# Optimization experiments

Measured on AMD Instinct MI355X. Metric: run time of the kernel, lower is better.

## Reference

```python
import jax, jax.numpy as jnp
import numpy as np

B, L, C = 8, 3136, 192
HEADS, HEAD_CH = 3, 64
EPS = 1e-5


def _dwconv(x, w, s):
    # depthwise 3x3 conv, SAME padding; w: [3,3,1,C], feature_group_count=C
    return jax.lax.conv_general_dilated(
        x, w, (s, s), 'SAME',
        dimension_numbers=('NHWC', 'HWIO', 'NHWC'),
        feature_group_count=x.shape[-1])


def _proj(x, dw, scale, bias, mean, var, pw, s):
    # depthwise conv -> BN (inference, running stats) -> 1x1 pointwise conv
    h = _dwconv(x, dw, s)
    h = (h - mean) * jax.lax.rsqrt(var + EPS) * scale + bias
    return jax.lax.conv_general_dilated(
        h, pw, (1, 1), 'SAME',
        dimension_numbers=('NHWC', 'HWIO', 'NHWC'))


def setup_inputs() -> dict:
    key = jax.random.key(0)
    ks = jax.random.split(key, 7)
    d = {'x': jax.random.normal(ks[0], (B, L, C), jnp.float32)}
    for i, p in enumerate(['q', 'k', 'v']):
        d[p + '_dw'] = jax.random.normal(ks[i + 1], (3, 3, 1, C), jnp.float32) * 0.1
        d[p + '_scale'] = jnp.ones((C,), jnp.float32)
        d[p + '_bias'] = jnp.zeros((C,), jnp.float32)
        d[p + '_mean'] = jnp.zeros((C,), jnp.float32)
        d[p + '_var'] = jnp.ones((C,), jnp.float32)
        d[p + '_pw'] = jax.random.normal(ks[i + 4], (1, 1, C, HEADS * HEAD_CH), jnp.float32) * 0.05
    d['is_training'] = 0  # inference: BN uses running averages
    return d


def reference(x, q_dw, q_scale, q_bias, q_mean, q_var, q_pw,
              k_dw, k_scale, k_bias, k_mean, k_var, k_pw,
              v_dw, v_scale, v_bias, v_mean, v_var, v_pw,
              is_training):
    S = int(np.ceil(np.sqrt(L)))  # 56; L is a perfect square, so no token padding
    xi = x.reshape(B, S, S, C)
    q = _proj(xi, q_dw, q_scale, q_bias, q_mean, q_var, q_pw, 1)  # [B,56,56,192]
    k = _proj(xi, k_dw, k_scale, k_bias, k_mean, k_var, k_pw, 2)  # [B,28,28,192]
    v = _proj(xi, v_dw, v_scale, v_bias, v_mean, v_var, v_pw, 2)  # [B,28,28,192]
    q = q.reshape(B, -1, HEADS, HEAD_CH) / jnp.sqrt(jnp.float32(HEAD_CH))
    k = k.reshape(B, -1, HEADS, HEAD_CH)
    v = v.reshape(B, -1, HEADS, HEAD_CH)
    attn = jax.nn.softmax(jnp.einsum('bqhd,bkhd->bhqk', q, k), axis=-1)
    o = jnp.einsum('bhqk,bkhd->bqhd', attn, v)
    # num_heads*head_ch == out_ch -> plain head merge, no output projection
    return o.reshape(B, L, HEADS * HEAD_CH)
```

## Files before the change

### kernel.cpp

```cpp
#include <hip/hip_runtime.h>
#include <cmath>

#define EPS_BN 1e-5f

typedef __bf16 bf16;
typedef __bf16 bf16x4 __attribute__((ext_vector_type(4)));
typedef __bf16 bf16x8 __attribute__((ext_vector_type(8)));
typedef float  f32x4  __attribute__((ext_vector_type(4)));

__device__ __forceinline__ void dma16(const bf16* g, bf16* l) {
    __builtin_amdgcn_global_load_lds(
        (const __attribute__((address_space(1))) void*)g,
        (__attribute__((address_space(3))) void*)l, 16, 0, 0);
}

__global__ __launch_bounds__(256) void conv_all_kernel(
    const float* __restrict__ x,
    const float* __restrict__ qdw, const float* __restrict__ qscale,
    const float* __restrict__ qbias, const float* __restrict__ qmean,
    const float* __restrict__ qvar,
    const float* __restrict__ kdw, const float* __restrict__ kscale,
    const float* __restrict__ kbias, const float* __restrict__ kmean,
    const float* __restrict__ kvar,
    const float* __restrict__ vdw, const float* __restrict__ vscale,
    const float* __restrict__ vbias, const float* __restrict__ vmean,
    const float* __restrict__ vvar,
    const float* __restrict__ qpw, const float* __restrict__ kpw,
    const float* __restrict__ vpw,
    bf16* __restrict__ qhi, bf16* __restrict__ qlo,
    bf16* __restrict__ khi, bf16* __restrict__ klo,
    bf16* __restrict__ vhi, bf16* __restrict__ vlo,
    bf16* __restrict__ wt) {
    const int WW = 56, C = 192;
    int bid = blockIdx.x;

    if (bid < 4704) {
        int idx = bid * 256 + threadIdx.x;
        int p  = idx / 48;
        int c4 = (idx - p * 48) * 4;
        int b  = p / 3136;
        int rem = p - b * 3136;
        int oy = rem / 56;
        int ox = rem - oy * 56;
        const float* xb = x + (size_t)b * 3136 * C;

        float4 sc = *(const float4*)&qscale[c4];
        float4 vr = *(const float4*)&qvar[c4];
        float4 bi = *(const float4*)&qbias[c4];
        float4 mn = *(const float4*)&qmean[c4];
        float aA[4] = {sc.x * rsqrtf(vr.x + EPS_BN), sc.y * rsqrtf(vr.y + EPS_BN),
                       sc.z * rsqrtf(vr.z + EPS_BN), sc.w * rsqrtf(vr.w + EPS_BN)};
        float aB[4] = {bi.x - mn.x * aA[0], bi.y - mn.y * aA[1],
                       bi.z - mn.z * aA[2], bi.w - mn.w * aA[3]};
        float s[4] = {0.f, 0.f, 0.f, 0.f};
#pragma unroll
        for (int ky = 0; ky < 3; ky++) {
            int iy = oy + ky - 1;
            bool yok = (iy >= 0) && (iy < 56);
#pragma unroll
            for (int kx = 0; kx < 3; kx++) {
                int ix = ox + kx - 1;
                if (yok && ix >= 0 && ix < WW) {
                    float4 xv = *(const float4*)&xb[((size_t)iy * WW + ix) * C + c4];
                    float4 wv = *(const float4*)&qdw[(ky * 3 + kx) * C + c4];
                    s[0] += xv.x * wv.x; s[1] += xv.y * wv.y;
                    s[2] += xv.z * wv.z; s[3] += xv.w * wv.w;
                }
            }
        }
        bf16x4 hv, lv;
#pragma unroll
        for (int j = 0; j < 4; j++) {
            float av = s[j] * aA[j] + aB[j];
            bf16 hh = (bf16)av;
            hv[j] = hh;
            lv[j] = (bf16)(av - (float)hh);
        }
        *(bf16x4*)&qhi[(size_t)p * C + c4] = hv;
        *(bf16x4*)&qlo[(size_t)p * C + c4] = lv;
    } else if (bid < 5880) {
        int idx = (bid - 4704) * 256 + threadIdx.x;
        int p  = idx / 48;
        int c4 = (idx - p * 48) * 4;
        int b  = p / 784;
        int rem = p - b * 784;
        int oy = rem / 28;
        int ox = rem - oy * 28;
        const float* xb = x + (size_t)b * 3136 * C;

        float ks[4] = {0.f, 0.f, 0.f, 0.f};
        float vs[4] = {0.f, 0.f, 0.f, 0.f};
#pragma unroll
        for (int ky = 0; ky < 3; ky++) {
            int iy = oy * 2 + ky;
            bool yok = iy < 56;
#pragma unroll
            for (int kx = 0; kx < 3; kx++) {
                int ix = ox * 2 + kx;
                if (yok && ix < WW) {
                    float4 xv = *(const float4*)&xb[((size_t)iy * WW + ix) * C + c4];
                    float4 kw = *(const float4*)&kdw[(ky * 3 + kx) * C + c4];
                    float4 vw = *(const float4*)&vdw[(ky * 3 + kx) * C + c4];
                    ks[0] += xv.x * kw.x; ks[1] += xv.y * kw.y;
                    ks[2] += xv.z * kw.z; ks[3] += xv.w * kw.w;
                    vs[0] += xv.x * vw.x; vs[1] += xv.y * vw.y;
                    vs[2] += xv.z * vw.z; vs[3] += xv.w * vw.w;
                }
            }
        }
        float4 ksc = *(const float4*)&kscale[c4];
        float4 kvr = *(const float4*)&kvar[c4];
        float4 kbi = *(const float4*)&kbias[c4];
        float4 kmn = *(const float4*)&kmean[c4];
        float4 vsc = *(const float4*)&vscale[c4];
        float4 vvr = *(const float4*)&vvar[c4];
        float4 vbi = *(const float4*)&vbias[c4];
        float4 vmn = *(const float4*)&vmean[c4];
        float kA[4] = {ksc.x * rsqrtf(kvr.x + EPS_BN), ksc.y * rsqrtf(kvr.y + EPS_BN),
                       ksc.z * rsqrtf(kvr.z + EPS_BN), ksc.w * rsqrtf(kvr.w + EPS_BN)};
        float kB[4] = {kbi.x - kmn.x * kA[0], kbi.y - kmn.y * kA[1],
                       kbi.z - kmn.z * kA[2], kbi.w - kmn.w * kA[3]};
        float vA[4] = {vsc.x * rsqrtf(vvr.x + EPS_BN), vsc.y * rsqrtf(vvr.y + EPS_BN),
                       vsc.z * rsqrtf(vvr.z + EPS_BN), vsc.w * rsqrtf(vvr.w + EPS_BN)};
        float vB[4] = {vbi.x - vmn.x * vA[0], vbi.y - vmn.y * vA[1],
                       vbi.z - vmn.z * vA[2], vbi.w - vmn.w * vA[3]};
        bf16x4 kh, kl, vh, vl;
#pragma unroll
        for (int j = 0; j < 4; j++) {
            float kf = ks[j] * kA[j] + kB[j];
            float vf = vs[j] * vA[j] + vB[j];
            bf16 h1 = (bf16)kf; kh[j] = h1; kl[j] = (bf16)(kf - (float)h1);
            bf16 h2 = (bf16)vf; vh[j] = h2; vl[j] = (bf16)(vf - (float)h2);
        }
        *(bf16x4*)&khi[(size_t)p * C + c4] = kh;
        *(bf16x4*)&klo[(size_t)p * C + c4] = kl;
        *(bf16x4*)&vhi[(size_t)p * C + c4] = vh;
        *(bf16x4*)&vlo[(size_t)p * C + c4] = vl;
    } else {
        int idx = (bid - 5880) * 256 + threadIdx.x;
        if (idx < 3 * 36864) {
            int mat = idx / 36864, r = idx % 36864;
            int n = r / 192, k = r - n * 192;
            const float* src = (mat == 0) ? qpw : (mat == 1) ? kpw : vpw;
            wt[idx] = (bf16)src[k * 192 + n];
        }
    }
}

__global__ __launch_bounds__(256) void gemm_all_kernel(
    const bf16* __restrict__ qhi, const bf16* __restrict__ qlo,
    const bf16* __restrict__ khi, const bf16* __restrict__ klo,
    const bf16* __restrict__ vhi, const bf16* __restrict__ vlo,
    const bf16* __restrict__ wt,
    bf16* __restrict__ qbuf, bf16* __restrict__ kbuf, bf16* __restrict__ vtbuf) {
    __shared__ bf16 Ws[192][200];
    int t = threadIdx.x;
    int bid = blockIdx.x;

    int mode, mt;
    const bf16 *Ahi, *Alo, *Wsrc;
    if (bid < 392)      { mode = 0; mt = bid;       Ahi = qhi; Alo = qlo; Wsrc = wt; }
    else if (bid < 490) { mode = 1; mt = bid - 392; Ahi = khi; Alo = klo; Wsrc = wt + 36864; }
    else                { mode = 2; mt = bid - 490; Ahi = vhi; Alo = vlo; Wsrc = wt + 73728; }

#pragma unroll
    for (int it = 0; it < 18; it++) {
        int idx = it * 256 + t;
        int n = idx / 24, ck = idx - n * 24;
        *(uint4*)&Ws[n][ck * 8] = *(const uint4*)&Wsrc[n * 192 + ck * 8];
    }
    __syncthreads();

    int lane = t & 63, wid = t >> 6;
    int l16 = lane & 15, quad = lane >> 4;
    int wrow = wid * 16;
    int m0 = mt * 64;

    f32x4 acc[12];
#pragma unroll
    for (int n = 0; n < 12; n++) acc[n] = f32x4{0.f, 0.f, 0.f, 0.f};

    const bf16* arh = Ahi + (size_t)(m0 + wrow + l16) * 192;
    const bf16* arl = Alo + (size_t)(m0 + wrow + l16) * 192;
#pragma unroll
    for (int kc = 0; kc < 6; kc++) {
        bf16x8 ah = *(const bf16x8*)(arh + kc * 32 + quad * 8);
        bf16x8 al = *(const bf16x8*)(arl + kc * 32 + quad * 8);
#pragma unroll
        for (int n = 0; n < 12; n++) {
            bf16x8 bfr = *(const bf16x8*)&Ws[n * 16 + l16][kc * 32 + quad * 8];
            acc[n] = __builtin_amdgcn_mfma_f32_16x16x32_bf16(al, bfr, acc[n], 0, 0, 0);
            acc[n] = __builtin_amdgcn_mfma_f32_16x16x32_bf16(ah, bfr, acc[n], 0, 0, 0);
        }
    }

    if (mode == 2) {
#pragma unroll
        for (int reg = 0; reg < 4; reg++) {
            int row = m0 + wrow + quad * 4 + reg;
            int b = row / 784;
            int loc = row - b * 784;
#pragma unroll
            for (int n = 0; n < 12; n++) {
                int col = n * 16 + l16;
                int h = col >> 6, d = col & 63;
                vtbuf[(((size_t)b * 3 + h) * 64 + d) * 784 + loc] = (bf16)acc[n][reg];
            }
        }
    } else {
        bf16* outp = (mode == 0) ? qbuf : kbuf;
        const float s = (mode == 0) ? 0.125f : 1.0f;
#pragma unroll
        for (int reg = 0; reg < 4; reg++) {
            size_t row = m0 + wrow + quad * 4 + reg;
#pragma unroll
            for (int n = 0; n < 12; n++)
                outp[row * 192 + n * 16 + l16] = (bf16)(acc[n][reg] * s);
        }
    }
}

__global__ __launch_bounds__(256)
__attribute__((amdgpu_waves_per_eu(3, 3)))
void attn3_kernel(const bf16* __restrict__ qb,
                  const bf16* __restrict__ kb,
                  const bf16* __restrict__ vtb,
                  float* __restrict__ out) {
    const int LQ = 3136, LK = 784, C = 192;
    int qt = blockIdx.x, h = blockIdx.y, b = blockIdx.z;

    __shared__ bf16 Ks[8192];
    __shared__ bf16 Vts[64][136];
    __shared__ bf16 Ps[64][136];

    int t    = threadIdx.x;
    int lane = t & 63;
    int wid  = t >> 6;
    int l16  = lane & 15;
    int quad = lane >> 4;
    int wrow = wid * 16;

    if (t < 128) {
        int row = t >> 1, part = t & 1;
        *(uint4*)&Ps[row][112 + part * 8] = make_uint4(0u, 0u, 0u, 0u);
    }

    bf16x8 qfrag[2];
    {
        const bf16* qrow = qb + ((size_t)b * LQ + qt * 64 + wrow + l16) * C + h * 64;
        qfrag[0] = *(const bf16x8*)(qrow + quad * 8);
        qfrag[1] = *(const bf16x8*)(qrow + 32 + quad * 8);
    }

    const bf16* kbase  = kb + (size_t)b * LK * C + h * 64;
    const bf16* vtbase = vtb + ((size_t)(b * 3 + h)) * 64 * LK;

    float m_run = -INFINITY, l_run = 0.f;
    f32x4 o_acc[4];
#pragma unroll
    for (int dt = 0; dt < 4; dt++) o_acc[dt] = f32x4{0.f, 0.f, 0.f, 0.f};

    for (int c = 0; c < 7; c++) {
        int j0 = c * 112;
        __syncthreads();

        for (int s = wid; s < 33; s += 4) {
            if (s < 16) {
                int j = s * 64 + lane;
                int r = j / 9, cc = j - r * 9;
                const bf16* src = (cc < 8 && r < 112)
                                  ? kbase + (size_t)(j0 + r) * C + cc * 8
                                  : kbase;
                dma16(src, &Ks[s * 512]);
            } else {
                int s2 = s - 16;
                int j = s2 * 64 + lane;
                int r = j / 17, cc = j - r * 17;
                const bf16* src = (cc < 14)
                                  ? vtbase + (size_t)r * LK + j0 + cc * 8
                                  : vtbase;
                dma16(src, (bf16*)Vts + s2 * 512);
            }
        }
        __syncthreads();

        f32x4 st[7];
#pragma unroll
        for (int kb7 = 0; kb7 < 7; kb7++) st[kb7] = f32x4{0.f, 0.f, 0.f, 0.f};
#pragma unroll
        for (int kk = 0; kk < 2; kk++) {
#pragma unroll
            for (int kb7 = 0; kb7 < 7; kb7++) {
                bf16x8 afrag = *(const bf16x8*)&Ks[(kb7 * 16 + l16) * 72 + kk * 32 + quad * 8];
                st[kb7] = __builtin_amdgcn_mfma_f32_16x16x32_bf16(afrag, qfrag[kk], st[kb7], 0, 0, 0);
            }
        }

        float mx = -INFINITY;
#pragma unroll
        for (int kb7 = 0; kb7 < 7; kb7++)
#pragma unroll
            for (int r = 0; r < 4; r++) mx = fmaxf(mx, st[kb7][r]);
        mx = fmaxf(mx, __shfl_xor(mx, 16, 64));
        mx = fmaxf(mx, __shfl_xor(mx, 32, 64));
        float m_new = fmaxf(m_run, mx);
        float alpha = __expf(m_run - m_new);

        float rs = 0.f;
#pragma unroll
        for (int kb7 = 0; kb7 < 7; kb7++) {
            bf16x4 pv;
#pragma unroll
            for (int r = 0; r < 4; r++) {
                float p = __expf(st[kb7][r] - m_new);
                rs += p;
                pv[r] = (bf16)p;
            }
            *(bf16x4*)&Ps[wrow + l16][kb7 * 16 + quad * 4] = pv;
        }
        rs += __shfl_xor(rs, 16, 64);
        rs += __shfl_xor(rs, 32, 64);
        l_run = l_run * alpha + rs;
        m_run = m_new;
#pragma unroll
        for (int dt = 0; dt < 4; dt++)
#pragma unroll
            for (int r = 0; r < 4; r++) o_acc[dt][r] *= alpha;

#pragma unroll
        for (int kk = 0; kk < 4; kk++) {
            bf16x8 pfrag = *(const bf16x8*)&Ps[wrow + l16][kk * 32 + quad * 8];
#pragma unroll
            for (int dt = 0; dt < 4; dt++) {
                bf16x8 vfrag = *(const bf16x8*)&Vts[dt * 16 + l16][kk * 32 + quad * 8];
                o_acc[dt] = __builtin_amdgcn_mfma_f32_16x16x32_bf16(vfrag, pfrag, o_acc[dt], 0, 0, 0);
            }
        }
    }

    float invl = 1.f / l_run;
    float* ob = out + ((size_t)b * LQ + qt * 64 + wrow + l16) * C + h * 64;
#pragma unroll
    for (int dt = 0; dt < 4; dt++) {
        float4 v4 = {o_acc[dt][0] * invl, o_acc[dt][1] * invl,
                     o_acc[dt][2] * invl, o_acc[dt][3] * invl};
        *(float4*)(ob + dt * 16 + quad * 4) = v4;
    }
}

extern "C" void kernel_launch(void* const* d_in, const int* in_sizes, int n_in,
                              void* d_out, int out_size, void* d_ws, size_t ws_size,
                              hipStream_t stream) {
    const float* x = (const float*)d_in[0];

    const float* q_dw = (const float*)d_in[1];
    const float* q_scale = (const float*)d_in[2];
    const float* q_bias = (const float*)d_in[3];
    const float* q_mean = (const float*)d_in[4];
    const float* q_var = (const float*)d_in[5];
    const float* q_pw = (const float*)d_in[6];

    const float* k_dw = (const float*)d_in[7];
    const float* k_scale = (const float*)d_in[8];
    const float* k_bias = (const float*)d_in[9];
    const float* k_mean = (const float*)d_in[10];
    const float* k_var = (const float*)d_in[11];
    const float* k_pw = (const float*)d_in[12];

    const float* v_dw = (const float*)d_in[13];
    const float* v_scale = (const float*)d_in[14];
    const float* v_bias = (const float*)d_in[15];
    const float* v_mean = (const float*)d_in[16];
    const float* v_var = (const float*)d_in[17];
    const float* v_pw = (const float*)d_in[18];

    float* out = (float*)d_out;

    char* ws = (char*)d_ws;
    bf16* qhi = (bf16*)(ws);
    bf16* qlo = (bf16*)(ws + 9633792);
    bf16* khi = (bf16*)(ws + 19267584);
    bf16* klo = (bf16*)(ws + 21676032);
    bf16* vhi = (bf16*)(ws + 24084480);
    bf16* vlo = (bf16*)(ws + 26492928);
    bf16* qbuf = (bf16*)(ws + 28901376);
    bf16* kbuf = (bf16*)(ws + 38535168);
    bf16* vtbuf = (bf16*)(ws + 40943616);
    bf16* wt = (bf16*)(ws + 43352064);

    conv_all_kernel<<<6312, 256, 0, stream>>>(
        x,
        q_dw, q_scale, q_bias, q_mean, q_var,
        k_dw, k_scale, k_bias, k_mean, k_var,
        v_dw, v_scale, v_bias, v_mean, v_var,
        q_pw, k_pw, v_pw,
        qhi, qlo, khi, klo, vhi, vlo, wt);

    gemm_all_kernel<<<588, 256, 0, stream>>>(
        qhi, qlo, khi, klo, vhi, vlo, wt, qbuf, kbuf, vtbuf);

    attn3_kernel<<<dim3(49, 3, 8), 256, 0, stream>>>(qbuf, kbuf, vtbuf, out);
}
```

Baseline: 187.1 us.

## Load K/V fragments directly from global memory and use exp2 softmax

The attention kernel no longer stages K and V^T tiles into shared memory with DMA loads and block barriers. Each wave now reads its MFMA operand fragments straight from global memory and relies on the caches for reuse across waves. The query scale is changed to fold log2(e) into it so the softmax can use exp2f. Occupancy is raised to 4 waves per EU because less LDS is needed. The cost is redundant global or L2 traffic, since all four waves reload the same K/V data with uncoalesced row-strided reads.

```diff
diff --git a/kernel.cpp b/kernel.cpp
--- a/kernel.cpp
+++ b/kernel.cpp
@@ -7,12 +7,6 @@
 typedef __bf16 bf16x4 __attribute__((ext_vector_type(4)));
 typedef __bf16 bf16x8 __attribute__((ext_vector_type(8)));
 typedef float  f32x4  __attribute__((ext_vector_type(4)));
-
-__device__ __forceinline__ void dma16(const bf16* g, bf16* l) {
-    __builtin_amdgcn_global_load_lds(
-        (const __attribute__((address_space(1))) void*)g,
-        (__attribute__((address_space(3))) void*)l, 16, 0, 0);
-}
 
 __global__ __launch_bounds__(256) void conv_all_kernel(
     const float* __restrict__ x,
@@ -209,7 +203,7 @@
         }
     } else {
         bf16* outp = (mode == 0) ? qbuf : kbuf;
-        const float s = (mode == 0) ? 0.125f : 1.0f;
+        const float s = (mode == 0) ? 0.18033688f : 1.0f;
 #pragma unroll
         for (int reg = 0; reg < 4; reg++) {
             size_t row = m0 + wrow + quad * 4 + reg;
@@ -221,16 +215,14 @@
 }
 
 __global__ __launch_bounds__(256)
-__attribute__((amdgpu_waves_per_eu(3, 3)))
-void attn3_kernel(const bf16* __restrict__ qb,
+__attribute__((amdgpu_waves_per_eu(4, 4)))
+void attn4_kernel(const bf16* __restrict__ qb,
                   const bf16* __restrict__ kb,
                   const bf16* __restrict__ vtb,
                   float* __restrict__ out) {
     const int LQ = 3136, LK = 784, C = 192;
     int qt = blockIdx.x, h = blockIdx.y, b = blockIdx.z;
 
-    __shared__ bf16 Ks[8192];
-    __shared__ bf16 Vts[64][136];
     __shared__ bf16 Ps[64][136];
 
     int t    = threadIdx.x;
@@ -240,9 +232,9 @@
     int quad = lane >> 4;
     int wrow = wid * 16;
 
-    if (t < 128) {
-        int row = t >> 1, part = t & 1;
-        *(uint4*)&Ps[row][112 + part * 8] = make_uint4(0u, 0u, 0u, 0u);
+    {
+        bf16x4 z = {(bf16)0.f, (bf16)0.f, (bf16)0.f, (bf16)0.f};
+        *(bf16x4*)&Ps[wrow + l16][112 + quad * 4] = z;
     }
 
     bf16x8 qfrag[2];
@@ -262,27 +254,6 @@
 
     for (int c = 0; c < 7; c++) {
         int j0 = c * 112;
-        __syncthreads();
-
-        for (int s = wid; s < 33; s += 4) {
-            if (s < 16) {
-                int j = s * 64 + lane;
-                int r = j / 9, cc = j - r * 9;
-                const bf16* src = (cc < 8 && r < 112)
-                                  ? kbase + (size_t)(j0 + r) * C + cc * 8
-                                  : kbase;
-                dma16(src, &Ks[s * 512]);
-            } else {
-                int s2 = s - 16;
-                int j = s2 * 64 + lane;
-                int r = j / 17, cc = j - r * 17;
-                const bf16* src = (cc < 14)
-                                  ? vtbase + (size_t)r * LK + j0 + cc * 8
-                                  : vtbase;
-                dma16(src, (bf16*)Vts + s2 * 512);
-            }
-        }
-        __syncthreads();
 
         f32x4 st[7];
 #pragma unroll
@@ -291,7 +262,7 @@
         for (int kk = 0; kk < 2; kk++) {
 #pragma unroll
             for (int kb7 = 0; kb7 < 7; kb7++) {
-                bf16x8 afrag = *(const bf16x8*)&Ks[(kb7 * 16 + l16) * 72 + kk * 32 + quad * 8];
+                bf16x8 afrag = *(const bf16x8*)(kbase + (size_t)(j0 + kb7 * 16 + l16) * C + kk * 32 + quad * 8);
                 st[kb7] = __builtin_amdgcn_mfma_f32_16x16x32_bf16(afrag, qfrag[kk], st[kb7], 0, 0, 0);
             }
         }
@@ -304,7 +275,7 @@
         mx = fmaxf(mx, __shfl_xor(mx, 16, 64));
         mx = fmaxf(mx, __shfl_xor(mx, 32, 64));
         float m_new = fmaxf(m_run, mx);
-        float alpha = __expf(m_run - m_new);
+        float alpha = exp2f(m_run - m_new);
 
         float rs = 0.f;
 #pragma unroll
@@ -312,7 +283,7 @@
             bf16x4 pv;
 #pragma unroll
             for (int r = 0; r < 4; r++) {
-                float p = __expf(st[kb7][r] - m_new);
+                float p = exp2f(st[kb7][r] - m_new);
                 rs += p;
                 pv[r] = (bf16)p;
             }
@@ -330,9 +301,11 @@
 #pragma unroll
         for (int kk = 0; kk < 4; kk++) {
             bf16x8 pfrag = *(const bf16x8*)&Ps[wrow + l16][kk * 32 + quad * 8];
+            int loc = kk * 32 + quad * 8;
+            int koff = (loc < 112) ? (j0 + loc) : 0;
 #pragma unroll
             for (int dt = 0; dt < 4; dt++) {
-                bf16x8 vfrag = *(const bf16x8*)&Vts[dt * 16 + l16][kk * 32 + quad * 8];
+                bf16x8 vfrag = *(const bf16x8*)(vtbase + (size_t)(dt * 16 + l16) * LK + koff);
                 o_acc[dt] = __builtin_amdgcn_mfma_f32_16x16x32_bf16(vfrag, pfrag, o_acc[dt], 0, 0, 0);
             }
         }
@@ -399,5 +372,5 @@
     gemm_all_kernel<<<588, 256, 0, stream>>>(
         qhi, qlo, khi, klo, vhi, vlo, wt, qbuf, kbuf, vtbuf);
 
-    attn3_kernel<<<dim3(49, 3, 8), 256, 0, stream>>>(qbuf, kbuf, vtbuf, out);
+    attn4_kernel<<<dim3(49, 3, 8), 256, 0, stream>>>(qbuf, kbuf, vtbuf, out);
 }
```

Measured after the change: 267.1 us. 42.8% more time.

## Process two query tiles per attention block to reuse K/V loads; use exp2

Applied to the files above, without the earlier changes.

Each attention block now handles up to two 64-row query tiles against every K/V chunk it loads into shared memory, halving the number of blocks and the K/V global-to-LDS traffic per query row. The Q scale folds in log2(e) so the softmax can use exp2f instead of __expf. The trade-offs are more register pressure from the doubled accumulators, fewer blocks (600) to spread across the GPU, and a tail block that handles only one tile.

```diff
diff --git a/kernel.cpp b/kernel.cpp
--- a/kernel.cpp
+++ b/kernel.cpp
@@ -209,7 +209,7 @@
         }
     } else {
         bf16* outp = (mode == 0) ? qbuf : kbuf;
-        const float s = (mode == 0) ? 0.125f : 1.0f;
+        const float s = (mode == 0) ? 0.18033688f : 1.0f;
 #pragma unroll
         for (int reg = 0; reg < 4; reg++) {
             size_t row = m0 + wrow + quad * 4 + reg;
@@ -222,12 +222,14 @@
 
 __global__ __launch_bounds__(256)
 __attribute__((amdgpu_waves_per_eu(3, 3)))
-void attn3_kernel(const bf16* __restrict__ qb,
+void attn5_kernel(const bf16* __restrict__ qb,
                   const bf16* __restrict__ kb,
                   const bf16* __restrict__ vtb,
                   float* __restrict__ out) {
     const int LQ = 3136, LK = 784, C = 192;
-    int qt = blockIdx.x, h = blockIdx.y, b = blockIdx.z;
+    int qp = blockIdx.x;
+    int h  = blockIdx.y, b = blockIdx.z;
+    int ntiles = (qp < 24) ? 2 : 1;
 
     __shared__ bf16 Ks[8192];
     __shared__ bf16 Vts[64][136];
@@ -245,20 +247,25 @@
         *(uint4*)&Ps[row][112 + part * 8] = make_uint4(0u, 0u, 0u, 0u);
     }
 
-    bf16x8 qfrag[2];
-    {
-        const bf16* qrow = qb + ((size_t)b * LQ + qt * 64 + wrow + l16) * C + h * 64;
-        qfrag[0] = *(const bf16x8*)(qrow + quad * 8);
-        qfrag[1] = *(const bf16x8*)(qrow + 32 + quad * 8);
+    bf16x8 qfrag[2][2];
+#pragma unroll
+    for (int tl = 0; tl < 2; tl++) {
+        int row = qp * 128 + ((tl < ntiles) ? tl : 0) * 64 + wrow + l16;
+        const bf16* qrow = qb + ((size_t)b * LQ + row) * C + h * 64;
+        qfrag[tl][0] = *(const bf16x8*)(qrow + quad * 8);
+        qfrag[tl][1] = *(const bf16x8*)(qrow + 32 + quad * 8);
     }
 
     const bf16* kbase  = kb + (size_t)b * LK * C + h * 64;
     const bf16* vtbase = vtb + ((size_t)(b * 3 + h)) * 64 * LK;
 
-    float m_run = -INFINITY, l_run = 0.f;
-    f32x4 o_acc[4];
-#pragma unroll
-    for (int dt = 0; dt < 4; dt++) o_acc[dt] = f32x4{0.f, 0.f, 0.f, 0.f};
+    float m_run[2] = {-INFINITY, -INFINITY};
+    float l_run[2] = {0.f, 0.f};
+    f32x4 o_acc[2][4];
+#pragma unroll
+    for (int tl = 0; tl < 2; tl++)
+#pragma unroll
+        for (int dt = 0; dt < 4; dt++) o_acc[tl][dt] = f32x4{0.f, 0.f, 0.f, 0.f};
 
     for (int c = 0; c < 7; c++) {
         int j0 = c * 112;
@@ -284,67 +291,71 @@
         }
         __syncthreads();
 
-        f32x4 st[7];
-#pragma unroll
-        for (int kb7 = 0; kb7 < 7; kb7++) st[kb7] = f32x4{0.f, 0.f, 0.f, 0.f};
-#pragma unroll
-        for (int kk = 0; kk < 2; kk++) {
+        for (int tl = 0; tl < ntiles; tl++) {
+            f32x4 st[7];
+#pragma unroll
+            for (int kb7 = 0; kb7 < 7; kb7++) st[kb7] = f32x4{0.f, 0.f, 0.f, 0.f};
+#pragma unroll
+            for (int kk = 0; kk < 2; kk++) {
+#pragma unroll
+                for (int kb7 = 0; kb7 < 7; kb7++) {
+                    bf16x8 afrag = *(const bf16x8*)&Ks[(kb7 * 16 + l16) * 72 + kk * 32 + quad * 8];
+                    st[kb7] = __builtin_amdgcn_mfma_f32_16x16x32_bf16(afrag, qfrag[tl][kk], st[kb7], 0, 0, 0);
+                }
+            }
+
+            float mx = -INFINITY;
+#pragma unroll
+            for (int kb7 = 0; kb7 < 7; kb7++)
+#pragma unroll
+                for (int r = 0; r < 4; r++) mx = fmaxf(mx, st[kb7][r]);
+            mx = fmaxf(mx, __shfl_xor(mx, 16, 64));
+            mx = fmaxf(mx, __shfl_xor(mx, 32, 64));
+            float m_new = fmaxf(m_run[tl], mx);
+            float alpha = exp2f(m_run[tl] - m_new);
+
+            float rs = 0.f;
 #pragma unroll
             for (int kb7 = 0; kb7 < 7; kb7++) {
-                bf16x8 afrag = *(const bf16x8*)&Ks[(kb7 * 16 + l16) * 72 + kk * 32 + quad * 8];
-                st[kb7] = __builtin_amdgcn_mfma_f32_16x16x32_bf16(afrag, qfrag[kk], st[kb7], 0, 0, 0);
-            }
-        }
-
-        float mx = -INFINITY;
-#pragma unroll
-        for (int kb7 = 0; kb7 < 7; kb7++)
-#pragma unroll
-            for (int r = 0; r < 4; r++) mx = fmaxf(mx, st[kb7][r]);
-        mx = fmaxf(mx, __shfl_xor(mx, 16, 64));
-        mx = fmaxf(mx, __shfl_xor(mx, 32, 64));
-        float m_new = fmaxf(m_run, mx);
-        float alpha = __expf(m_run - m_new);
-
-        float rs = 0.f;
-#pragma unroll
-        for (int kb7 = 0; kb7 < 7; kb7++) {
-            bf16x4 pv;
-#pragma unroll
-            for (int r = 0; r < 4; r++) {
-                float p = __expf(st[kb7][r] - m_new);
-                rs += p;
-                pv[r] = (bf16)p;
-            }
-            *(bf16x4*)&Ps[wrow + l16][kb7 * 16 + quad * 4] = pv;
-        }
-        rs += __shfl_xor(rs, 16, 64);
-        rs += __shfl_xor(rs, 32, 64);
-        l_run = l_run * alpha + rs;
-        m_run = m_new;
-#pragma unroll
-        for (int dt = 0; dt < 4; dt++)
-#pragma unroll
-            for (int r = 0; r < 4; r++) o_acc[dt][r] *= alpha;
-
-#pragma unroll
-        for (int kk = 0; kk < 4; kk++) {
-            bf16x8 pfrag = *(const bf16x8*)&Ps[wrow + l16][kk * 32 + quad * 8];
-#pragma unroll
-            for (int dt = 0; dt < 4; dt++) {
-                bf16x8 vfrag = *(const bf16x8*)&Vts[dt * 16 + l16][kk * 32 + quad * 8];
-                o_acc[dt] = __builtin_amdgcn_mfma_f32_16x16x32_bf16(vfrag, pfrag, o_acc[dt], 0, 0, 0);
-            }
-        }
-    }
-
-    float invl = 1.f / l_run;
-    float* ob = out + ((size_t)b * LQ + qt * 64 + wrow + l16) * C + h * 64;
-#pragma unroll
-    for (int dt = 0; dt < 4; dt++) {
-        float4 v4 = {o_acc[dt][0] * invl, o_acc[dt][1] * invl,
-                     o_acc[dt][2] * invl, o_acc[dt][3] * invl};
-        *(float4*)(ob + dt * 16 + quad * 4) = v4;
+                bf16x4 pv;
+#pragma unroll
+                for (int r = 0; r < 4; r++) {
+                    float p = exp2f(st[kb7][r] - m_new);
+                    rs += p;
+                    pv[r] = (bf16)p;
+                }
+                *(bf16x4*)&Ps[wrow + l16][kb7 * 16 + quad * 4] = pv;
+            }
+            rs += __shfl_xor(rs, 16, 64);
+            rs += __shfl_xor(rs, 32, 64);
+            l_run[tl] = l_run[tl] * alpha + rs;
+            m_run[tl] = m_new;
+#pragma unroll
+            for (int dt = 0; dt < 4; dt++)
+#pragma unroll
+                for (int r = 0; r < 4; r++) o_acc[tl][dt][r] *= alpha;
+
+#pragma unroll
+            for (int kk = 0; kk < 4; kk++) {
+                bf16x8 pfrag = *(const bf16x8*)&Ps[wrow + l16][kk * 32 + quad * 8];
+#pragma unroll
+                for (int dt = 0; dt < 4; dt++) {
+                    bf16x8 vfrag = *(const bf16x8*)&Vts[dt * 16 + l16][kk * 32 + quad * 8];
+                    o_acc[tl][dt] = __builtin_amdgcn_mfma_f32_16x16x32_bf16(vfrag, pfrag, o_acc[tl][dt], 0, 0, 0);
+                }
+            }
+        }
+    }
+
+    for (int tl = 0; tl < ntiles; tl++) {
+        float invl = 1.f / l_run[tl];
+        float* ob = out + ((size_t)b * LQ + qp * 128 + tl * 64 + wrow + l16) * C + h * 64;
+#pragma unroll
+        for (int dt = 0; dt < 4; dt++) {
+            float4 v4 = {o_acc[tl][dt][0] * invl, o_acc[tl][dt][1] * invl,
+                         o_acc[tl][dt][2] * invl, o_acc[tl][dt][3] * invl};
+            *(float4*)(ob + dt * 16 + quad * 4) = v4;
+        }
     }
 }
 
@@ -399,5 +410,5 @@
     gemm_all_kernel<<<588, 256, 0, stream>>>(
         qhi, qlo, khi, klo, vhi, vlo, wt, qbuf, kbuf, vtbuf);
 
-    attn3_kernel<<<dim3(49, 3, 8), 256, 0, stream>>>(qbuf, kbuf, vtbuf, out);
+    attn5_kernel<<<dim3(25, 3, 8), 256, 0, stream>>>(qbuf, kbuf, vtbuf, out);
 }
```

New measurement: 260.3 us. 39.1% more time.
